# Performance work log

Measured on AMD Instinct MI355X. Metric: run time of the kernel, lower is better.

Reference implementation:

```python
import jax, jax.numpy as jnp
import numpy as np

N_NODES = 100000
N_EDGES = 3200000
IN_DIM = 11
HID = 32


def setup_inputs() -> dict:
    key = jax.random.key(0)
    ks = jax.random.split(key, 12)
    inp = {
        "x": jax.random.normal(ks[0], (N_NODES, IN_DIM), dtype=jnp.float32),
        "edge_index": jax.random.randint(ks[1], (2, N_EDGES), 0, N_NODES, dtype=jnp.int32),
        "batch": jnp.zeros((N_NODES,), dtype=jnp.int32),
        # GCNConv layer 1 (11 -> 32)
        "W1": jax.random.normal(ks[2], (IN_DIM, HID), dtype=jnp.float32) / np.sqrt(IN_DIM),
        "b1": jnp.zeros((HID,), dtype=jnp.float32),
        # GCNConv layer 2 (32 -> 32)
        "W2": jax.random.normal(ks[3], (HID, HID), dtype=jnp.float32) / np.sqrt(HID),
        "b2": jnp.zeros((HID,), dtype=jnp.float32),
        # output MLP: 32 -> 16 -> 1
        "Wo1": jax.random.normal(ks[4], (HID, HID // 2), dtype=jnp.float32) / np.sqrt(HID),
        "bo1": jnp.zeros((HID // 2,), dtype=jnp.float32),
        "Wo2": jax.random.normal(ks[5], (HID // 2, 1), dtype=jnp.float32) / np.sqrt(HID // 2),
        "bo2": jnp.zeros((1,), dtype=jnp.float32),
    }
    return inp


def _gcn_norm(edge_index, n_nodes):
    # Add self-loops and compute symmetric normalization (PyG GCNConv default).
    loops = jnp.arange(n_nodes, dtype=edge_index.dtype)
    src = jnp.concatenate([edge_index[0], loops])
    dst = jnp.concatenate([edge_index[1], loops])
    ones = jnp.ones_like(dst, dtype=jnp.float32)
    deg = jax.ops.segment_sum(ones, dst, num_segments=n_nodes)  # degree of A+I on target side
    dinv = jax.lax.rsqrt(deg)  # deg >= 1 thanks to self-loops
    norm = dinv[src] * dinv[dst]  # [E+N]
    return src, dst, norm


def _gcn_conv(x, W, b, src, dst, norm, n_nodes):
    xw = x @ W                                   # transform first (small dim)
    msg = norm[:, None] * xw[src]                # gather + scale  [E+N, H]
    agg = jax.ops.segment_sum(msg, dst, num_segments=n_nodes)  # scatter-add
    return agg + b


def reference(x, edge_index, batch, W1, b1, W2, b2, Wo1, bo1, Wo2, bo2):
    n = x.shape[0]
    src, dst, norm = _gcn_norm(edge_index, n)
    h = jax.nn.relu(_gcn_conv(x, W1, b1, src, dst, norm, n))
    # F.dropout(training=self.training) is identity in eval mode
    h = jax.nn.relu(_gcn_conv(h, W2, b2, src, dst, norm, n))
    h = jax.nn.elu(h @ Wo1 + bo1)
    out = h @ Wo2 + bo2
    return out.squeeze(-1)  # [N]
```

## Files before the change

kernel.cpp:

```cpp
#include <hip/hip_runtime.h>
#include <hip/hip_fp16.h>
#include <math.h>

#define N_NODES 100000
#define N_EDGES 3200000
#define IN_DIM 11
#define HID 32
#define HID2 16
#define SCHUNK 100352
#define BINSHIFT 8
#define BINSZ 256
#define NB 391
#define CHUNK 4096
#define NCH 782

__device__ __forceinline__ int wincl(int v) {
    int lane = threadIdx.x & 63;
#pragma unroll
    for (int d = 1; d < 64; d <<= 1) {
        int u = __shfl_up(v, d, 64);
        v += (lane >= d) ? u : 0;
    }
    return v;
}

__device__ __forceinline__ int blkexcl512(int v, int* wtot) {
    int t = threadIdx.x, lane = t & 63, w = t >> 6;
    int inc = wincl(v);
    if (lane == 63) wtot[w] = inc;
    __syncthreads();
    if (t < 8) {
        int x = wtot[t], ix = x;
#pragma unroll
        for (int d = 1; d < 8; d <<= 1) {
            int u = __shfl_up(ix, d, 64);
            ix += (lane >= d) ? u : 0;
        }
        wtot[t] = ix - x;
    }
    __syncthreads();
    return inc - v + wtot[w];
}

__global__ __launch_bounds__(256) void k_hist(const int* __restrict__ ei,
                                              int* __restrict__ cnthist) {
    __shared__ int h[NB];
    int t = threadIdx.x;
    for (int i = t; i < NB; i += 256) h[i] = 0;
    __syncthreads();
    int b0 = blockIdx.x * CHUNK;
    int n = N_EDGES - b0; if (n > CHUNK) n = CHUNK;
    for (int e = t * 4; e < n; e += 1024) {
        int4 d4 = *(const int4*)(ei + N_EDGES + b0 + e);
        atomicAdd(&h[d4.x >> BINSHIFT], 1);
        atomicAdd(&h[d4.y >> BINSHIFT], 1);
        atomicAdd(&h[d4.z >> BINSHIFT], 1);
        atomicAdd(&h[d4.w >> BINSHIFT], 1);
    }
    __syncthreads();
    for (int i = t; i < NB; i += 256)
        cnthist[i * NCH + blockIdx.x] = h[i];
}

__global__ __launch_bounds__(256) void k_colscan(int* __restrict__ cnthist,
                                                 int* __restrict__ colsum) {
    __shared__ int wtot[4];
    int i = blockIdx.x;
    int t = threadIdx.x;
    int lane = t & 63;
    int v[4];
    int s4 = 0;
#pragma unroll
    for (int u = 0; u < 4; ++u) {
        int idx = t * 4 + u;
        v[u] = (idx < NCH) ? cnthist[i * NCH + idx] : 0;
        s4 += v[u];
    }
    int inc = wincl(s4);
    if (lane == 63) wtot[t >> 6] = inc;
    __syncthreads();
    if (t < 4) {
        int x = wtot[t], ix = x;
#pragma unroll
        for (int d = 1; d < 4; d <<= 1) {
            int u2 = __shfl_up(ix, d, 64);
            ix += (lane >= d) ? u2 : 0;
        }
        wtot[t] = ix - x;
    }
    __syncthreads();
    int base = inc - s4 + wtot[t >> 6];
#pragma unroll
    for (int u = 0; u < 4; ++u) {
        int idx = t * 4 + u;
        if (idx < NCH) cnthist[i * NCH + idx] = base;
        base += v[u];
    }
    if (t == 255) colsum[i] = base;
}

__global__ __launch_bounds__(512) void k_scanbins(const int* __restrict__ colsum,
                                                  int* __restrict__ binbase) {
    __shared__ int wtot[8];
    int t = threadIdx.x;
    int v = (t < NB) ? colsum[t] : 0;
    int pre = blkexcl512(v, wtot);
    if (t < NB) binbase[t] = pre;
    if (t == 0) binbase[NB] = N_EDGES;
}

__global__ __launch_bounds__(512) void k_binscatter(const int* __restrict__ ei,
                                                    const int* __restrict__ binbase,
                                                    const int* __restrict__ cnthist,
                                                    unsigned* __restrict__ binbuf) {
    __shared__ unsigned short sbin[CHUNK];
    __shared__ unsigned char  sdl[CHUNK];
    __shared__ unsigned       srecS[CHUNK];
    __shared__ unsigned short sbinS[CHUNK];
    __shared__ int h[NB], rl[NB], gb[NB];
    __shared__ int wtot[8];
    int t = threadIdx.x;
    int b0 = blockIdx.x * CHUNK;
    int n = N_EDGES - b0; if (n > CHUNK) n = CHUNK;
    for (int i = t; i < NB; i += 512) h[i] = 0;
    __syncthreads();
    for (int e = t; e < n; e += 512) {
        int d = ei[N_EDGES + b0 + e];
        int b = d >> BINSHIFT;
        sbin[e] = (unsigned short)b;
        sdl[e]  = (unsigned char)(d & (BINSZ - 1));
        atomicAdd(&h[b], 1);
    }
    __syncthreads();
    int c = (t < NB) ? h[t] : 0;
    int pre = blkexcl512(c, wtot);
    if (t < NB) {
        rl[t] = pre;
        gb[t] = binbase[t] + cnthist[t * NCH + blockIdx.x];
        h[t] = 0;
    }
    __syncthreads();
    for (int e = t; e < n; e += 512) {
        int s = ei[b0 + e];
        int b = sbin[e];
        int p = rl[b] + atomicAdd(&h[b], 1);
        srecS[p] = (unsigned)s | ((unsigned)sdl[e] << 17);
        sbinS[p] = (unsigned short)b;
    }
    __syncthreads();
    for (int p = t; p < n; p += 512) {
        int b = sbinS[p];
        binbuf[gb[b] + (p - rl[b])] = srecS[p];
    }
}

__global__ __launch_bounds__(512) void k_binfill(const unsigned* __restrict__ binbuf,
                                                 const int* __restrict__ binbase,
                                                 int* __restrict__ rowstart,
                                                 float* __restrict__ dinv,
                                                 int* __restrict__ csr_src) {
    int bb = blockIdx.x;
    int b = bb >> 1;
    int half = bb & 1;
    int t = threadIdx.x;
    __shared__ int cnt[BINSZ], rloc[BINSZ], cur[BINSZ], wtot[8];
    int ebeg = binbase[b], eend = binbase[b + 1];
    if (t < BINSZ) cnt[t] = 0;
    __syncthreads();
    for (int e = ebeg + t; e < eend; e += 512)
        atomicAdd(&cnt[binbuf[e] >> 17], 1);
    __syncthreads();
    int c = (t < BINSZ) ? cnt[t] : 0;
    int pre = blkexcl512(c, wtot);
    if (t < BINSZ) {
        rloc[t] = pre;
        cur[t] = 0;
        int node = b * BINSZ + t;
        if ((t >> 7) == half && node < N_NODES) {
            rowstart[node] = ebeg + pre;
            dinv[node] = rsqrtf((float)c + 1.0f);
        }
    }
    if (bb == 0 && t == 0) rowstart[N_NODES] = N_EDGES;
    __syncthreads();
    for (int e = ebeg + t; e < eend; e += 512) {
        unsigned vv = binbuf[e];
        int dl = vv >> 17;
        if ((dl >> 7) == half) {
            int p = ebeg + rloc[dl] + atomicAdd(&cur[dl], 1);
            csr_src[p] = (int)(vv & 0x1FFFFu);
        }
    }
}

__global__ void k_xw1(const float* __restrict__ x, const float* __restrict__ W1,
                      const float* __restrict__ dinv, __half* __restrict__ xwh) {
    int t = blockIdx.x * blockDim.x + threadIdx.x;
    int node = t >> 5;
    int j = t & 31;
    __shared__ float sW[IN_DIM * HID];
    __shared__ float sx[8 * IN_DIM];
    for (int i = threadIdx.x; i < IN_DIM * HID; i += 256) sW[i] = W1[i];
    int base = blockIdx.x * 8;
    if (threadIdx.x < 8 * IN_DIM) sx[threadIdx.x] = x[base * IN_DIM + threadIdx.x];
    __syncthreads();
    int ln = node - base;
    float acc = 0.0f;
#pragma unroll
    for (int k = 0; k < IN_DIM; ++k)
        acc += sx[ln * IN_DIM + k] * sW[k * HID + j];
    xwh[t] = __float2half(dinv[node] * acc);
}

__device__ __forceinline__ void accum8(float* __restrict__ acc, const uint4 v) {
    float2 f0 = __half22float2(*(const __half2*)&v.x);
    float2 f1 = __half22float2(*(const __half2*)&v.y);
    float2 f2 = __half22float2(*(const __half2*)&v.z);
    float2 f3 = __half22float2(*(const __half2*)&v.w);
    acc[0] += f0.x; acc[1] += f0.y;
    acc[2] += f1.x; acc[3] += f1.y;
    acc[4] += f2.x; acc[5] += f2.y;
    acc[6] += f3.x; acc[7] += f3.y;
}

__device__ __forceinline__ void edge_accum8(int beg, int end, int q, int oj,
                                            const int* __restrict__ csr_src,
                                            const __half* __restrict__ xwh,
                                            float* __restrict__ acc) {
#pragma unroll
    for (int k = 0; k < 8; ++k) acc[k] = 0.0f;
    int e = beg;
    for (; e + 32 <= end; e += 32) {
        int s0 = csr_src[e + q];
        int s1 = csr_src[e + 8 + q];
        int s2 = csr_src[e + 16 + q];
        int s3 = csr_src[e + 24 + q];
        uint4 v0 = *(const uint4*)(xwh + ((s0 << 5) | oj));
        uint4 v1 = *(const uint4*)(xwh + ((s1 << 5) | oj));
        uint4 v2 = *(const uint4*)(xwh + ((s2 << 5) | oj));
        uint4 v3 = *(const uint4*)(xwh + ((s3 << 5) | oj));
        accum8(acc, v0); accum8(acc, v1); accum8(acc, v2); accum8(acc, v3);
    }
    if (e + 16 <= end) {
        int s0 = csr_src[e + q];
        int s1 = csr_src[e + 8 + q];
        uint4 v0 = *(const uint4*)(xwh + ((s0 << 5) | oj));
        uint4 v1 = *(const uint4*)(xwh + ((s1 << 5) | oj));
        accum8(acc, v0); accum8(acc, v1);
        e += 16;
    }
    if (e + 8 <= end) {
        int s0 = csr_src[e + q];
        uint4 v0 = *(const uint4*)(xwh + ((s0 << 5) | oj));
        accum8(acc, v0);
        e += 8;
    }
    if (e + q < end) {
        int s0 = csr_src[e + q];
        uint4 v0 = *(const uint4*)(xwh + ((s0 << 5) | oj));
        accum8(acc, v0);
    }
#pragma unroll
    for (int m = 4; m <= 16; m <<= 1) {
#pragma unroll
        for (int k = 0; k < 8; ++k) acc[k] += __shfl_xor(acc[k], m);
    }
}

__global__ __launch_bounds__(256) void k_gather_xw2(const int* __restrict__ rowstart,
                                                    const float* __restrict__ dinv,
                                                    const int* __restrict__ csr_src,
                                                    const __half* __restrict__ xwh1,
                                                    const float* __restrict__ b1,
                                                    const float* __restrict__ W2,
                                                    __half* __restrict__ xwh2) {
    __shared__ float sW2[HID * HID];
    __shared__ float sA[8][33];
    __shared__ float sH[8][33];
    for (int i = threadIdx.x; i < HID * HID; i += 256) sW2[i] = W2[i];

    int ln = threadIdx.x >> 5;
    int node = blockIdx.x * 8 + ln;
    int l = threadIdx.x & 31;
    int q = l >> 2;
    int oj = (l & 3) << 3;

    float acc[8];
    edge_accum8(rowstart[node], rowstart[node + 1], q, oj, csr_src, xwh1, acc);
    if (q == 0) {
#pragma unroll
        for (int k = 0; k < 8; ++k) sA[ln][oj + k] = acc[k];
    }
    __syncthreads();

    int j = l;
    float dd = dinv[node];
    float hv = dd * (sA[ln][j] + __half2float(xwh1[node * HID + j])) + b1[j];
    sH[ln][j] = hv > 0.0f ? hv : 0.0f;
    __syncthreads();

    float a2 = 0.0f;
#pragma unroll
    for (int k = 0; k < HID; ++k) a2 += sH[ln][k] * sW2[k * HID + j];
    xwh2[node * HID + j] = __float2half(dd * a2);
}

__global__ __launch_bounds__(256) void k_gather_mlp(const int* __restrict__ rowstart,
                                                    const float* __restrict__ dinv,
                                                    const int* __restrict__ csr_src,
                                                    const __half* __restrict__ xwh,
                                                    const float* __restrict__ b2,
                                                    const float* __restrict__ Wo1,
                                                    const float* __restrict__ bo1,
                                                    const float* __restrict__ Wo2,
                                                    const float* __restrict__ bo2,
                                                    float* __restrict__ out) {
    __shared__ float sW1[HID * HID2];
    __shared__ float sb1[HID2];
    __shared__ float sW2v[HID2];
    __shared__ float sb2[HID];
    __shared__ float sA[8][33];
    __shared__ float sH[8][33];
    for (int i = threadIdx.x; i < HID * HID2; i += 256) sW1[i] = Wo1[i];
    if (threadIdx.x < HID2) {
        sb1[threadIdx.x] = bo1[threadIdx.x];
        sW2v[threadIdx.x] = Wo2[threadIdx.x];
    }
    if (threadIdx.x < HID) sb2[threadIdx.x] = b2[threadIdx.x];

    int ln = threadIdx.x >> 5;
    int node = blockIdx.x * 8 + ln;
    int l = threadIdx.x & 31;
    int q = l >> 2;
    int oj = (l & 3) << 3;

    float acc[8];
    edge_accum8(rowstart[node], rowstart[node + 1], q, oj, csr_src, xwh, acc);
    if (q == 0) {
#pragma unroll
        for (int k = 0; k < 8; ++k) sA[ln][oj + k] = acc[k];
    }
    __syncthreads();

    int j = l;
    float dd = dinv[node];
    float hv = dd * (sA[ln][j] + __half2float(xwh[node * HID + j])) + sb2[j];
    sH[ln][j] = hv > 0.0f ? hv : 0.0f;
    __syncthreads();

    float val = 0.0f;
    if (j < HID2) {
        float a = sb1[j];
#pragma unroll
        for (int k = 0; k < HID; ++k) a += sH[ln][k] * sW1[k * HID2 + j];
        a = a > 0.0f ? a : (expf(a) - 1.0f);
        val = a * sW2v[j];
    }
#pragma unroll
    for (int d = 16; d >= 1; d >>= 1) val += __shfl_down(val, d, 32);
    if (j == 0) out[node] = val + bo2[0];
}

extern "C" void kernel_launch(void* const* d_in, const int* in_sizes, int n_in,
                              void* d_out, int out_size, void* d_ws, size_t ws_size,
                              hipStream_t stream) {
    const float* x   = (const float*)d_in[0];
    const int*   ei  = (const int*)d_in[1];
    const float* W1  = (const float*)d_in[3];
    const float* b1  = (const float*)d_in[4];
    const float* W2  = (const float*)d_in[5];
    const float* b2  = (const float*)d_in[6];
    const float* Wo1 = (const float*)d_in[7];
    const float* bo1 = (const float*)d_in[8];
    const float* Wo2 = (const float*)d_in[9];
    const float* bo2 = (const float*)d_in[10];
    float* out = (float*)d_out;

    int*      colsum   = (int*)d_ws;
    int*      binbase  = colsum + 512;
    int*      rowstart = binbase + 512;
    float*    dinv     = (float*)(rowstart + SCHUNK);
    int*      csr_src  = (int*)(dinv + SCHUNK);
    unsigned* binbuf   = (unsigned*)(csr_src + N_EDGES);
    __half*   XWH1     = (__half*)(binbuf + N_EDGES);
    __half*   XWH2     = XWH1 + (size_t)N_NODES * HID;
    int*      cnthist  = csr_src;

    const int BT = 256;
    int gNH  = (N_NODES * HID + BT - 1) / BT;
    int gG   = N_NODES / 8;

    k_hist      <<<NCH, BT, 0, stream>>>(ei, cnthist);
    k_colscan   <<<NB, BT, 0, stream>>>(cnthist, colsum);
    k_scanbins  <<<1, 512, 0, stream>>>(colsum, binbase);
    k_binscatter<<<NCH, 512, 0, stream>>>(ei, binbase, cnthist, binbuf);
    k_binfill   <<<2 * NB, 512, 0, stream>>>(binbuf, binbase, rowstart, dinv, csr_src);

    k_xw1<<<gNH, BT, 0, stream>>>(x, W1, dinv, XWH1);
    k_gather_xw2<<<gG, BT, 0, stream>>>(rowstart, dinv, csr_src, XWH1, b1, W2, XWH2);

    k_gather_mlp<<<gG, BT, 0, stream>>>(rowstart, dinv, csr_src, XWH2,
                                        b2, Wo1, bo1, Wo2, bo2, out);
}
```

Baseline: 250.6 us.

## Reuse colscan offsets in binscatter and cache bin records in LDS

Chunk size grows from 4096 to 6144 edges, so fewer chunk blocks are launched. k_colscan now also writes each bin's total as an extra column, which lets k_binscatter compute per-chunk bin counts from the scanned prefix table. That removes its own histogram pass, one barrier and the staging arrays. k_binfill keeps up to 9216 bin records in shared memory so the second pass skips a global re-read, at the cost of more LDS per block and possibly lower occupancy.

```diff
diff --git a/kernel.cpp b/kernel.cpp
--- a/kernel.cpp
+++ b/kernel.cpp
@@ -11,8 +11,10 @@
 #define BINSHIFT 8
 #define BINSZ 256
 #define NB 391
-#define CHUNK 4096
-#define NCH 782
+#define CHUNK 6144
+#define NCH 521
+#define NCH1 522
+#define FCAP 9216
 
 __device__ __forceinline__ int wincl(int v) {
     int lane = threadIdx.x & 63;
@@ -59,7 +61,7 @@
     }
     __syncthreads();
     for (int i = t; i < NB; i += 256)
-        cnthist[i * NCH + blockIdx.x] = h[i];
+        cnthist[i * NCH1 + blockIdx.x] = h[i];
 }
 
 __global__ __launch_bounds__(256) void k_colscan(int* __restrict__ cnthist,
@@ -73,7 +75,7 @@
 #pragma unroll
     for (int u = 0; u < 4; ++u) {
         int idx = t * 4 + u;
-        v[u] = (idx < NCH) ? cnthist[i * NCH + idx] : 0;
+        v[u] = (idx < NCH) ? cnthist[i * NCH1 + idx] : 0;
         s4 += v[u];
     }
     int inc = wincl(s4);
@@ -93,10 +95,13 @@
 #pragma unroll
     for (int u = 0; u < 4; ++u) {
         int idx = t * 4 + u;
-        if (idx < NCH) cnthist[i * NCH + idx] = base;
+        if (idx < NCH) cnthist[i * NCH1 + idx] = base;
         base += v[u];
     }
-    if (t == 255) colsum[i] = base;
+    if (t == 255) {
+        cnthist[i * NCH1 + NCH] = base;
+        colsum[i] = base;
+    }
 }
 
 __global__ __launch_bounds__(512) void k_scanbins(const int* __restrict__ colsum,
@@ -113,8 +118,6 @@
                                                     const int* __restrict__ binbase,
                                                     const int* __restrict__ cnthist,
                                                     unsigned* __restrict__ binbuf) {
-    __shared__ unsigned short sbin[CHUNK];
-    __shared__ unsigned char  sdl[CHUNK];
     __shared__ unsigned       srecS[CHUNK];
     __shared__ unsigned short sbinS[CHUNK];
     __shared__ int h[NB], rl[NB], gb[NB];
@@ -122,29 +125,24 @@
     int t = threadIdx.x;
     int b0 = blockIdx.x * CHUNK;
     int n = N_EDGES - b0; if (n > CHUNK) n = CHUNK;
-    for (int i = t; i < NB; i += 512) h[i] = 0;
+    int pre_b = 0, c = 0;
+    if (t < NB) {
+        pre_b = cnthist[t * NCH1 + blockIdx.x];
+        c = cnthist[t * NCH1 + blockIdx.x + 1] - pre_b;
+    }
+    int rlv = blkexcl512(c, wtot);
+    if (t < NB) {
+        rl[t] = rlv;
+        gb[t] = binbase[t] + pre_b;
+        h[t] = 0;
+    }
     __syncthreads();
     for (int e = t; e < n; e += 512) {
         int d = ei[N_EDGES + b0 + e];
+        int s = ei[b0 + e];
         int b = d >> BINSHIFT;
-        sbin[e] = (unsigned short)b;
-        sdl[e]  = (unsigned char)(d & (BINSZ - 1));
-        atomicAdd(&h[b], 1);
-    }
-    __syncthreads();
-    int c = (t < NB) ? h[t] : 0;
-    int pre = blkexcl512(c, wtot);
-    if (t < NB) {
-        rl[t] = pre;
-        gb[t] = binbase[t] + cnthist[t * NCH + blockIdx.x];
-        h[t] = 0;
-    }
-    __syncthreads();
-    for (int e = t; e < n; e += 512) {
-        int s = ei[b0 + e];
-        int b = sbin[e];
         int p = rl[b] + atomicAdd(&h[b], 1);
-        srecS[p] = (unsigned)s | ((unsigned)sdl[e] << 17);
+        srecS[p] = (unsigned)s | ((unsigned)(d & (BINSZ - 1)) << 17);
         sbinS[p] = (unsigned short)b;
     }
     __syncthreads();
@@ -163,12 +161,17 @@
     int b = bb >> 1;
     int half = bb & 1;
     int t = threadIdx.x;
+    __shared__ unsigned srec[FCAP];
     __shared__ int cnt[BINSZ], rloc[BINSZ], cur[BINSZ], wtot[8];
     int ebeg = binbase[b], eend = binbase[b + 1];
+    int m = eend - ebeg;
     if (t < BINSZ) cnt[t] = 0;
     __syncthreads();
-    for (int e = ebeg + t; e < eend; e += 512)
-        atomicAdd(&cnt[binbuf[e] >> 17], 1);
+    for (int e = t; e < m; e += 512) {
+        unsigned v = binbuf[ebeg + e];
+        if (e < FCAP) srec[e] = v;
+        atomicAdd(&cnt[v >> 17], 1);
+    }
     __syncthreads();
     int c = (t < BINSZ) ? cnt[t] : 0;
     int pre = blkexcl512(c, wtot);
@@ -183,8 +186,8 @@
     }
     if (bb == 0 && t == 0) rowstart[N_NODES] = N_EDGES;
     __syncthreads();
-    for (int e = ebeg + t; e < eend; e += 512) {
-        unsigned vv = binbuf[e];
+    for (int e = t; e < m; e += 512) {
+        unsigned vv = (e < FCAP) ? srec[e] : binbuf[ebeg + e];
         int dl = vv >> 17;
         if ((dl >> 7) == half) {
             int p = ebeg + rloc[dl] + atomicAdd(&cur[dl], 1);
```

After: 239.4 us. -4.4%, faster.
